# Optimization experiments

Measured on AMD Instinct MI355X. Metric: run time of the kernel, lower is better.

## Reference

```python
import jax, jax.numpy as jnp
import numpy as np

NEG_SLOPE = 0.2  # HANConv default negative_slope
N_NODES = 100000
N_REL = 8
N_EDGES = 200000
N_LABEL = 131072
C_IN = 128
H1 = 128
H2 = 128


def _segment_softmax(logits, seg, num_segments):
    # PyG softmax(src, index): exp(src - max_per_seg) / (sum_per_seg + 1e-16)
    m = jax.ops.segment_max(logits, seg, num_segments=num_segments)
    m = jnp.where(jnp.isfinite(m), m, 0.0)  # empty segments -> 0
    e = jnp.exp(logits - m[seg])
    s = jax.ops.segment_sum(e, seg, num_segments=num_segments)
    return e / (s[seg] + 1e-16)


def _han_layer(x, edge_index, proj_w, proj_b, att_src, att_dst, q, klin_w, klin_b):
    # x: [N, Cin]; edge_index: [R, 2, E]; att_src/att_dst: [R, D]; klin_w: [D, D] (torch [out,in])
    N = x.shape[0]
    h = x @ proj_w + proj_b            # [N, D] shared projection for node type 'node'
    a_src = h @ att_src.T              # [N, R] per-node src attention logits
    a_dst = h @ att_dst.T              # [N, R]

    def per_rel(eidx, a_s, a_d):
        src, dst = eidx[0], eidx[1]
        alpha = jax.nn.leaky_relu(a_s[src] + a_d[dst], NEG_SLOPE)     # [E]
        alpha = _segment_softmax(alpha, dst, N)                        # softmax over in-neighbors
        out = jax.ops.segment_sum(alpha[:, None] * h[src], dst, num_segments=N)  # [N, D]
        return jax.nn.relu(out)        # HANConv applies relu per edge-type output

    outs = jax.vmap(per_rel, in_axes=(0, 1, 1))(edge_index, a_src, a_dst)  # [R, N, D]
    # semantic attention across edge types (group())
    score = jnp.einsum('d,rd->r', q, jnp.tanh(outs @ klin_w.T + klin_b).mean(axis=1))
    attn = jax.nn.softmax(score)       # [R]
    return jnp.einsum('r,rnd->nd', attn, outs)


def setup_inputs() -> dict:
    key = jax.random.key(0)
    ks = jax.random.split(key, 24)
    f32 = jnp.float32

    def lin_w(k, fin, fout):
        return (jax.random.normal(k, (fin, fout), f32) / np.sqrt(fin)).astype(f32)

    inp = {
        'x': jax.random.normal(ks[0], (N_NODES, C_IN), f32),
        'edge_index': jax.random.randint(ks[1], (N_REL, 2, N_EDGES), 0, N_NODES, jnp.int32),
        'edge_label_index': jax.random.randint(ks[2], (2, N_LABEL), 0, N_NODES, jnp.int32),
        # HANConv layer 1 params
        'w1': lin_w(ks[3], C_IN, H1), 'b1': jnp.zeros((H1,), f32),
        'asrc1': jax.random.normal(ks[4], (N_REL, H1), f32) / np.sqrt(H1),
        'adst1': jax.random.normal(ks[5], (N_REL, H1), f32) / np.sqrt(H1),
        'q1': jax.random.normal(ks[6], (H1,), f32) / np.sqrt(H1),
        'kw1': lin_w(ks[7], H1, H1).T, 'kb1': jnp.zeros((H1,), f32),
        # HANConv layer 2 params
        'w2': lin_w(ks[8], H1, H2), 'b2': jnp.zeros((H2,), f32),
        'asrc2': jax.random.normal(ks[9], (N_REL, H2), f32) / np.sqrt(H2),
        'adst2': jax.random.normal(ks[10], (N_REL, H2), f32) / np.sqrt(H2),
        'q2': jax.random.normal(ks[11], (H2,), f32) / np.sqrt(H2),
        'kw2': lin_w(ks[12], H2, H2).T, 'kb2': jnp.zeros((H2,), f32),
        # link-score head
        'post_w': lin_w(ks[13], H2, 2), 'post_b': jnp.zeros((2,), f32),
    }
    return inp


def reference(x, edge_index, edge_label_index,
              w1, b1, asrc1, adst1, q1, kw1, kb1,
              w2, b2, asrc2, adst2, q2, kw2, kb2,
              post_w, post_b):
    h = jax.nn.relu(_han_layer(x, edge_index, w1, b1, asrc1, adst1, q1, kw1, kb1))
    h = jax.nn.relu(_han_layer(h, edge_index, w2, b2, asrc2, adst2, q2, kw2, kb2))
    h_had = h[edge_label_index[0]] * h[edge_label_index[1]]   # [L, H2]
    logits = h_had @ post_w + post_b                          # [L, 2]
    return logits.sum(axis=-1)                                # [L]
```

## Files before the change

kernel.cpp:

```cpp
#include <hip/hip_runtime.h>

#define NN 100000
#define NR 8
#define NE 200000
#define NL 131072
#define NSEG (NR*NN)
#define NB_SCAN 782
#define NPAD (NB_SCAN*1024)

typedef __attribute__((ext_vector_type(8))) short short8;
typedef __attribute__((ext_vector_type(8))) _Float16 half8;
typedef __attribute__((ext_vector_type(4))) float floatx4;

__device__ __forceinline__ unsigned short f2h(float f) {
    _Float16 h = (_Float16)f;
    union { _Float16 h; unsigned short u; } c; c.h = h; return c.u;
}
__device__ __forceinline__ float h2f(unsigned short u) {
    union { _Float16 h; unsigned short u; } c; c.u = u; return (float)c.h;
}

__global__ void transpose128(const float* __restrict__ in, float* __restrict__ out) {
    int idx = blockIdx.x * 256 + threadIdx.x;
    int j = idx >> 7, k = idx & 127;
    out[idx] = in[k * 128 + j];
}

__global__ void cast_f16(const float* __restrict__ src, unsigned short* __restrict__ dst) {
    size_t idx = ((size_t)blockIdx.x * 256 + threadIdx.x) * 4;
    float4 v = *(const float4*)(src + idx);
    ushort4 o;
    o.x = f2h(v.x); o.y = f2h(v.y); o.z = f2h(v.z); o.w = f2h(v.w);
    *(ushort4*)(dst + idx) = o;
}

__global__ void hist_kernel(const int* __restrict__ ei, int* __restrict__ counts) {
    int idx = blockIdx.x * 256 + threadIdx.x;
    if (idx >= NR * NE) return;
    int r = idx / NE, e = idx - r * NE;
    int dst = ei[(size_t)r * 2 * NE + NE + e];
    atomicAdd(&counts[r * NN + dst], 1);
}

__global__ __launch_bounds__(256) void scan_k1(const int* __restrict__ counts,
                                               int* __restrict__ rowptr,
                                               int* __restrict__ bsums) {
    __shared__ int wsum[4];
    int t = threadIdx.x, lane = t & 63, w = t >> 6;
    int base = blockIdx.x * 1024 + t * 4;
    int c0 = counts[base], c1 = counts[base + 1], c2 = counts[base + 2], c3 = counts[base + 3];
    int s = c0 + c1 + c2 + c3;
    int inc = s;
#pragma unroll
    for (int off = 1; off < 64; off <<= 1) { int v = __shfl_up(inc, off); if (lane >= off) inc += v; }
    if (lane == 63) wsum[w] = inc;
    __syncthreads();
    int wbase = 0;
    for (int k = 0; k < w; ++k) wbase += wsum[k];
    int ex = wbase + inc - s;
    rowptr[base]     = ex;
    rowptr[base + 1] = ex + c0;
    rowptr[base + 2] = ex + c0 + c1;
    rowptr[base + 3] = ex + c0 + c1 + c2;
    if (t == 255) bsums[blockIdx.x] = wbase + inc;
}

__global__ __launch_bounds__(256) void scan_k2(int* __restrict__ bsums, int nb) {
    __shared__ int wsum[4];
    __shared__ int carry_s;
    int t = threadIdx.x, lane = t & 63, w = t >> 6;
    if (t == 0) carry_s = 0;
    __syncthreads();
    for (int base = 0; base < nb; base += 256) {
        int i = base + t;
        int v = (i < nb) ? bsums[i] : 0;
        int inc = v;
#pragma unroll
        for (int off = 1; off < 64; off <<= 1) { int u = __shfl_up(inc, off); if (lane >= off) inc += u; }
        if (lane == 63) wsum[w] = inc;
        __syncthreads();
        int wbase = carry_s;
        for (int k = 0; k < w; ++k) wbase += wsum[k];
        if (i < nb) bsums[i] = wbase + inc - v;
        __syncthreads();
        if (t == 0) carry_s += wsum[0] + wsum[1] + wsum[2] + wsum[3];
        __syncthreads();
    }
}

__global__ void scan_k3(int* __restrict__ rowptr, const int* __restrict__ bsums) {
    int i = blockIdx.x * 256 + threadIdx.x;
    if (i <= NSEG) rowptr[i] += bsums[i >> 10];
}

__global__ void fill_kernel(const int* __restrict__ ei, const int* __restrict__ rowptr,
                            int* __restrict__ cursor, int* __restrict__ es_raw) {
    int idx = blockIdx.x * 256 + threadIdx.x;
    if (idx >= NR * NE) return;
    int r = idx / NE, e = idx - r * NE;
    int src = ei[(size_t)r * 2 * NE + e];
    int dst = ei[(size_t)r * 2 * NE + NE + e];
    int g = r * NN + dst;
    int pos = rowptr[g] + atomicAdd(&cursor[g], 1);
    es_raw[2 * pos] = src;
}

__global__ __launch_bounds__(256, 3) void gemm_proj(
    const float* __restrict__ A, const float* __restrict__ B,
    const float* __restrict__ bias, float* __restrict__ out, int nrows)
{
    __shared__ float As[128][36];
    __shared__ float Bs[128][36];
    const int tid = threadIdx.x;
    const int row0 = blockIdx.x * 128;
    const int cg = tid & 15;
    const int nb = (tid >> 4) * 8;

    float acc[8][8];
#pragma unroll
    for (int i = 0; i < 8; ++i)
#pragma unroll
        for (int j = 0; j < 8; ++j) acc[i][j] = 0.f;

    for (int k0 = 0; k0 < 128; k0 += 32) {
#pragma unroll
        for (int i = 0; i < 4; ++i) {
            int fi = tid + i * 256;
            int rw = fi >> 3, kq = fi & 7;
            int n = row0 + rw;
            float4 v = make_float4(0.f, 0.f, 0.f, 0.f);
            if (n < nrows) v = *(const float4*)(A + (size_t)n * 128 + k0 + kq * 4);
            *(float4*)&As[rw][kq * 4] = v;
            float4 w = *(const float4*)(B + rw * 128 + k0 + kq * 4);
            *(float4*)&Bs[rw][kq * 4] = w;
        }
        __syncthreads();
#pragma unroll 2
        for (int kq = 0; kq < 8; ++kq) {
            float4 wv[8];
#pragma unroll
            for (int j = 0; j < 8; ++j) wv[j] = *(const float4*)&Bs[cg + 16 * j][kq * 4];
#pragma unroll
            for (int i = 0; i < 8; ++i) {
                float4 xv = *(const float4*)&As[nb + i][kq * 4];
#pragma unroll
                for (int j = 0; j < 8; ++j)
                    acc[i][j] += xv.x * wv[j].x + xv.y * wv[j].y
                               + xv.z * wv[j].z + xv.w * wv[j].w;
            }
        }
        __syncthreads();
    }
#pragma unroll
    for (int i = 0; i < 8; ++i) {
        int n = row0 + nb + i;
        if (n < nrows) {
#pragma unroll
            for (int j = 0; j < 8; ++j) {
                int d = cg + 16 * j;
                out[(size_t)n * 128 + d] = acc[i][j] + bias[d];
            }
        }
    }
}

__global__ __launch_bounds__(256) void fused_score2(
    const int* __restrict__ rowptr, const int2* __restrict__ es,
    const unsigned short* __restrict__ h16,
    const unsigned short* __restrict__ kw16, const float* __restrict__ kb,
    const float* __restrict__ q, float* __restrict__ scorebuf)
{
    __shared__ unsigned short Os[64][136];
    __shared__ float redbuf[4];
    const int t = threadIdx.x;
    const int r = blockIdx.y;
    const int row0 = blockIdx.x * 64;
    const int l = t & 7, ng = t >> 3;

#pragma unroll
    for (int pass = 0; pass < 2; ++pass) {
        int nl = pass * 32 + ng;
        int n = row0 + nl;
        float acc[16];
#pragma unroll
        for (int i = 0; i < 16; ++i) acc[i] = 0.f;
        if (n < NN) {
            int g = r * NN + n;
            int p0 = rowptr[g], p1 = rowptr[g + 1];
            int e = p0;
            for (; e + 1 < p1; e += 2) {
                int2 ea = es[e], eb = es[e + 1];
                float aa = __int_as_float(ea.y), ab = __int_as_float(eb.y);
                const unsigned short* hpa = h16 + (size_t)ea.x * 128;
                const unsigned short* hpb = h16 + (size_t)eb.x * 128;
                short8 a0 = *(const short8*)(hpa + l * 8);
                short8 a1 = *(const short8*)(hpa + 64 + l * 8);
                short8 b0 = *(const short8*)(hpb + l * 8);
                short8 b1 = *(const short8*)(hpb + 64 + l * 8);
#pragma unroll
                for (int i = 0; i < 8; ++i)
                    acc[i]     += aa * h2f((unsigned short)a0[i]) + ab * h2f((unsigned short)b0[i]);
#pragma unroll
                for (int i = 0; i < 8; ++i)
                    acc[8 + i] += aa * h2f((unsigned short)a1[i]) + ab * h2f((unsigned short)b1[i]);
            }
            if (e < p1) {
                int2 ea = es[e];
                float aa = __int_as_float(ea.y);
                const unsigned short* hpa = h16 + (size_t)ea.x * 128;
                short8 a0 = *(const short8*)(hpa + l * 8);
                short8 a1 = *(const short8*)(hpa + 64 + l * 8);
#pragma unroll
                for (int i = 0; i < 8; ++i) acc[i]     += aa * h2f((unsigned short)a0[i]);
#pragma unroll
                for (int i = 0; i < 8; ++i) acc[8 + i] += aa * h2f((unsigned short)a1[i]);
            }
        }
        unsigned short ov[16];
#pragma unroll
        for (int i = 0; i < 16; ++i) ov[i] = f2h(fmaxf(acc[i], 0.f));
        *(short8*)&Os[nl][l * 8]      = *(short8*)&ov[0];
        *(short8*)&Os[nl][64 + l * 8] = *(short8*)&ov[8];
    }
    __syncthreads();

    const int wave = t >> 6, lane = t & 63;
    const int quad = lane >> 4, l16 = lane & 15;
    half8 a[4];
#pragma unroll
    for (int kc = 0; kc < 4; ++kc)
        a[kc] = *(const half8*)&Os[wave * 16 + l16][quad * 8 + kc * 32];

    float s = 0.f;
#pragma unroll
    for (int dt = 0; dt < 8; ++dt) {
        const unsigned short* brow = kw16 + (size_t)(dt * 16 + l16) * 128 + quad * 8;
        floatx4 accv = {0.f, 0.f, 0.f, 0.f};
#pragma unroll
        for (int kc = 0; kc < 4; ++kc) {
            half8 b = *(const half8*)(brow + kc * 32);
            accv = __builtin_amdgcn_mfma_f32_16x16x32_f16(a[kc], b, accv, 0, 0, 0);
        }
        int d = dt * 16 + l16;
        float kbv = kb[d], qv = q[d];
#pragma unroll
        for (int reg = 0; reg < 4; ++reg) {
            int node = row0 + wave * 16 + quad * 4 + reg;
            if (node < NN) {
                float y = accv[reg] + kbv;
                float e2 = __expf(2.f * y);
                float tn = 1.f - 2.f * __builtin_amdgcn_rcpf(e2 + 1.f);
                s += tn * qv;
            }
        }
    }
    for (int off = 32; off > 0; off >>= 1) s += __shfl_down(s, off);
    if (lane == 0) redbuf[wave] = s;
    __syncthreads();
    if (t == 0) atomicAdd(scorebuf + r * 64 + (blockIdx.x & 63),
                          redbuf[0] + redbuf[1] + redbuf[2] + redbuf[3]);
}

__global__ void score_reduce(const float* __restrict__ scorebuf, float* __restrict__ score) {
    int t = threadIdx.x;
    int r = t >> 3, k = t & 7;
    float v = 0.f;
#pragma unroll
    for (int i = 0; i < 8; ++i) v += scorebuf[r * 64 + k * 8 + i];
    v += __shfl_down(v, 4);
    v += __shfl_down(v, 2);
    v += __shfl_down(v, 1);
    if (k == 0) score[r] = v;
}

__global__ __launch_bounds__(256) void att_kernel(
    const float* __restrict__ h, const float* __restrict__ asrc_w,
    const float* __restrict__ adst_w, float* __restrict__ a_src,
    float* __restrict__ a_dst, unsigned short* __restrict__ h16)
{
    __shared__ float hs[16][128];
    int n0 = blockIdx.x * 16;
#pragma unroll
    for (int i = 0; i < 2; ++i) {
        int fi = threadIdx.x + i * 256;
        int n = fi >> 5, kq = fi & 31;
        float4 v = make_float4(0.f, 0.f, 0.f, 0.f);
        if (n0 + n < NN) v = *(const float4*)(h + (size_t)(n0 + n) * 128 + kq * 4);
        *(float4*)&hs[n][kq * 4] = v;
    }
    __syncthreads();
    int n = threadIdx.x >> 4, rr = threadIdx.x & 15;
    int r = rr & 7; int isd = rr >> 3;
    const float* w = (isd ? adst_w : asrc_w) + r * 128;
    float acc = 0.f;
#pragma unroll
    for (int kq = 0; kq < 32; ++kq) {
        float4 hv = *(const float4*)&hs[n][kq * 4];
        float4 wv = ((const float4*)w)[kq];
        acc += hv.x * wv.x + hv.y * wv.y + hv.z * wv.z + hv.w * wv.w;
    }
    if (n0 + n < NN) (isd ? a_dst : a_src)[r * NN + n0 + n] = acc;

    int dq = rr * 8;
    if (n0 + n < NN) {
        unsigned short ov[8];
#pragma unroll
        for (int k = 0; k < 8; ++k) ov[k] = f2h(hs[n][dq + k]);
        *(short8*)(h16 + (size_t)(n0 + n) * 128 + dq) = *(short8*)ov;
    }
}

__global__ void softmax_csr(const int* __restrict__ rowptr, int2* __restrict__ es,
                            const float* __restrict__ a_src, const float* __restrict__ a_dst)
{
    int g = blockIdx.x * 256 + threadIdx.x;
    if (g >= NSEG) return;
    int p0 = rowptr[g], p1 = rowptr[g + 1];
    if (p0 == p1) return;
    int r = g / NN;
    float ad = a_dst[g];
    const float* as = a_src + (size_t)r * NN;
    float m = -1e30f;
    int i = p0;
    for (; i + 1 < p1; i += 2) {
        float la = as[es[i].x] + ad;
        float lb = as[es[i + 1].x] + ad;
        la = la > 0.f ? la : 0.2f * la;
        lb = lb > 0.f ? lb : 0.2f * lb;
        es[i].y     = __float_as_int(la);
        es[i + 1].y = __float_as_int(lb);
        m = fmaxf(m, fmaxf(la, lb));
    }
    if (i < p1) {
        float la = as[es[i].x] + ad;
        la = la > 0.f ? la : 0.2f * la;
        es[i].y = __float_as_int(la);
        m = fmaxf(m, la);
    }
    float s = 0.f;
    for (int k = p0; k < p1; ++k) {
        float e = __expf(__int_as_float(es[k].y) - m);
        es[k].y = __float_as_int(e);
        s += e;
    }
    float inv = __builtin_amdgcn_rcpf(s + 1e-16f);
    for (int k = p0; k < p1; ++k)
        es[k].y = __float_as_int(__int_as_float(es[k].y) * inv);
}

__global__ __launch_bounds__(256) void combine_csr(
    const int* __restrict__ rowptr, const int2* __restrict__ es,
    const unsigned short* __restrict__ h16, const float* __restrict__ score,
    float* __restrict__ comb)
{
    __shared__ float attn[NR];
    __shared__ float lds[4][64][17];
    int t = threadIdx.x;
    if (t == 0) {
        float sc[NR]; float m = -1e30f;
        for (int r = 0; r < NR; ++r) { sc[r] = score[r] * (1.0f / NN); m = fmaxf(m, sc[r]); }
        float den = 0.f;
        for (int r = 0; r < NR; ++r) { sc[r] = __expf(sc[r] - m); den += sc[r]; }
        for (int r = 0; r < NR; ++r) attn[r] = sc[r] / den;
    }
    __syncthreads();

    int nl = t >> 6;
    int n = blockIdx.x * 4 + nl;
    int L = t & 63;
    int r = L >> 3;
    int o = L & 7;
    float a[16];
#pragma unroll
    for (int i = 0; i < 16; ++i) a[i] = 0.f;
    {
        int g = r * NN + n;
        int p0 = rowptr[g], p1 = rowptr[g + 1];
        int e = p0;
        for (; e + 1 < p1; e += 2) {
            int2 ea = es[e], eb = es[e + 1];
            float aa = __int_as_float(ea.y), ab = __int_as_float(eb.y);
            const unsigned short* hpa = h16 + (size_t)ea.x * 128;
            const unsigned short* hpb = h16 + (size_t)eb.x * 128;
            short8 u0 = *(const short8*)(hpa + o * 8);
            short8 u1 = *(const short8*)(hpa + 64 + o * 8);
            short8 v0 = *(const short8*)(hpb + o * 8);
            short8 v1 = *(const short8*)(hpb + 64 + o * 8);
#pragma unroll
            for (int i = 0; i < 8; ++i) {
                a[i]     += aa * h2f((unsigned short)u0[i]) + ab * h2f((unsigned short)v0[i]);
                a[8 + i] += aa * h2f((unsigned short)u1[i]) + ab * h2f((unsigned short)v1[i]);
            }
        }
        if (e < p1) {
            int2 ea = es[e];
            float aa = __int_as_float(ea.y);
            const unsigned short* hpa = h16 + (size_t)ea.x * 128;
            short8 u0 = *(const short8*)(hpa + o * 8);
            short8 u1 = *(const short8*)(hpa + 64 + o * 8);
#pragma unroll
            for (int i = 0; i < 8; ++i) {
                a[i]     += aa * h2f((unsigned short)u0[i]);
                a[8 + i] += aa * h2f((unsigned short)u1[i]);
            }
        }
    }
    float w = attn[r];
    float* dst = &lds[nl][L][0];
#pragma unroll
    for (int i = 0; i < 16; ++i) dst[i] = w * fmaxf(a[i], 0.f);
    __syncthreads();

    int d0 = 2 * L;
    int o2, s0;
    if (d0 < 64) { o2 = d0 >> 3; s0 = d0 & 7; }
    else         { o2 = (d0 - 64) >> 3; s0 = 8 + ((d0 - 64) & 7); }
    float x0 = 0.f, x1 = 0.f;
#pragma unroll
    for (int rr = 0; rr < NR; ++rr) {
        x0 += lds[nl][rr * 8 + o2][s0];
        x1 += lds[nl][rr * 8 + o2][s0 + 1];
    }
    *(float2*)(comb + (size_t)n * 128 + d0) = make_float2(x0, x1);
}

__global__ __launch_bounds__(256) void head_kernel(
    const float* __restrict__ hfin, const int* __restrict__ eli,
    const float* __restrict__ pw, const float* __restrict__ pb,
    float* __restrict__ out)
{
    int t = threadIdx.x;
    int l = blockIdx.x * 4 + (t >> 6);
    int d0 = (t & 63) * 2;
    int a = eli[l], b = eli[NL + l];
    float2 ha = *(const float2*)(hfin + (size_t)a * 128 + d0);
    float2 hb = *(const float2*)(hfin + (size_t)b * 128 + d0);
    float w0 = pw[d0 * 2] + pw[d0 * 2 + 1];
    float w1 = pw[d0 * 2 + 2] + pw[d0 * 2 + 3];
    float v = ha.x * hb.x * w0 + ha.y * hb.y * w1;
    for (int off = 32; off > 0; off >>= 1) v += __shfl_down(v, off);
    if ((t & 63) == 0) out[l] = v + pb[0] + pb[1];
}

extern "C" void kernel_launch(void* const* d_in, const int* in_sizes, int n_in,
                              void* d_out, int out_size, void* d_ws, size_t ws_size,
                              hipStream_t stream)
{
    const float* x     = (const float*)d_in[0];
    const int*   ei    = (const int*)d_in[1];
    const int*   eli   = (const int*)d_in[2];
    const float* w1    = (const float*)d_in[3];
    const float* b1    = (const float*)d_in[4];
    const float* asrc1 = (const float*)d_in[5];
    const float* adst1 = (const float*)d_in[6];
    const float* q1    = (const float*)d_in[7];
    const float* kw1   = (const float*)d_in[8];
    const float* kb1   = (const float*)d_in[9];
    const float* w2    = (const float*)d_in[10];
    const float* b2    = (const float*)d_in[11];
    const float* asrc2 = (const float*)d_in[12];
    const float* adst2 = (const float*)d_in[13];
    const float* q2    = (const float*)d_in[14];
    const float* kw2   = (const float*)d_in[15];
    const float* kb2   = (const float*)d_in[16];
    const float* pw    = (const float*)d_in[17];
    const float* pb    = (const float*)d_in[18];
    float* out = (float*)d_out;

    float* ws      = (float*)d_ws;
    float* hA      = ws;
    float* hB      = ws + 12800000ull;
    float* a_src   = ws + 25600000ull;
    float* a_dst   = ws + 26400000ull;
    int2*  es      = (int2*)(ws + 27200000ull);
    int*   rowptr  = (int*)(ws + 30400000ull);
    int*   counts  = (int*)(ws + 31200768ull);
    int*   bsums   = (int*)(ws + 32001536ull);
    float* score   = ws + 32002560ull;
    float* wt      = ws + 32002624ull;
    unsigned short* kw16 = (unsigned short*)(ws + 32019008ull);
    float* scorebuf = (float*)counts;

    hipMemsetAsync(counts, 0, NPAD * sizeof(int), stream);
    hist_kernel<<<6250, 256, 0, stream>>>(ei, counts);
    scan_k1<<<NB_SCAN, 256, 0, stream>>>(counts, rowptr, bsums);
    scan_k2<<<1, 256, 0, stream>>>(bsums, NB_SCAN);
    scan_k3<<<3126, 256, 0, stream>>>(rowptr, bsums);
    hipMemsetAsync(counts, 0, NPAD * sizeof(int), stream);
    fill_kernel<<<6250, 256, 0, stream>>>(ei, rowptr, counts, (int*)es);

    for (int layer = 0; layer < 2; ++layer) {
        const float* Ain  = layer ? hA : x;
        float*       H    = layer ? hB : hA;
        unsigned short* h16 = (unsigned short*)(layer ? hA : hB);
        const float* W    = layer ? w2 : w1;
        const float* bb   = layer ? b2 : b1;
        const float* as_w = layer ? asrc2 : asrc1;
        const float* ad_w = layer ? adst2 : adst1;
        const float* qq   = layer ? q2 : q1;
        const float* kw   = layer ? kw2 : kw1;
        const float* kb   = layer ? kb2 : kb1;

        transpose128<<<64, 256, 0, stream>>>(W, wt);
        gemm_proj<<<782, 256, 0, stream>>>(Ain, wt, bb, H, NN);
        cast_f16<<<16, 256, 0, stream>>>(kw, kw16);
        att_kernel<<<6250, 256, 0, stream>>>(H, as_w, ad_w, a_src, a_dst, h16);
        softmax_csr<<<3125, 256, 0, stream>>>(rowptr, es, a_src, a_dst);
        hipMemsetAsync(scorebuf, 0, 512 * sizeof(float), stream);
        fused_score2<<<dim3(1563, NR), 256, 0, stream>>>(rowptr, es, h16,
                                                         kw16, kb, qq, scorebuf);
        score_reduce<<<1, 64, 0, stream>>>(scorebuf, score);
        combine_csr<<<25000, 256, 0, stream>>>(rowptr, es, h16, score, H);
    }
    head_kernel<<<32768, 256, 0, stream>>>(hB, eli, pw, pb, out);
}
```

Before: 1.305 ms.

## Gather FP8 node features in semantic score kernel and register-cache softmax logits

The attention kernel now also writes an FP8 e4m3 copy of the projected features, and the semantic-score aggregation gathers 16 FP8 bytes per lane instead of 32 FP16 bytes. This halves gather traffic in that kernel and changes the per-lane column mapping to contiguous 16-element chunks. The segment softmax keeps up to 16 logits in registers, so it no longer does repeated read-modify-write passes over the edge array for low-degree segments. The cost is reduced precision in the semantic attention scores and an extra FP8 store in the attention kernel.

```diff
diff --git a/kernel.cpp b/kernel.cpp
--- a/kernel.cpp
+++ b/kernel.cpp
@@ -1,4 +1,5 @@
 #include <hip/hip_runtime.h>
+#include <hip/hip_fp8.h>
 
 #define NN 100000
 #define NR 8
@@ -18,6 +19,12 @@
 }
 __device__ __forceinline__ float h2f(unsigned short u) {
     union { _Float16 h; unsigned short u; } c; c.u = u; return (float)c.h;
+}
+__device__ __forceinline__ unsigned fp8enc(float f) {
+    __hip_fp8_e4m3 t(f); return (unsigned)t.__x;
+}
+__device__ __forceinline__ float fp8dec(unsigned b) {
+    __hip_fp8_e4m3 t; t.__x = (__hip_fp8_storage_t)b; return (float)t;
 }
 
 __global__ void transpose128(const float* __restrict__ in, float* __restrict__ out) {
@@ -166,7 +173,7 @@
 
 __global__ __launch_bounds__(256) void fused_score2(
     const int* __restrict__ rowptr, const int2* __restrict__ es,
-    const unsigned short* __restrict__ h16,
+    const unsigned char* __restrict__ h8,
     const unsigned short* __restrict__ kw16, const float* __restrict__ kb,
     const float* __restrict__ q, float* __restrict__ scorebuf)
 {
@@ -191,36 +198,34 @@
             for (; e + 1 < p1; e += 2) {
                 int2 ea = es[e], eb = es[e + 1];
                 float aa = __int_as_float(ea.y), ab = __int_as_float(eb.y);
-                const unsigned short* hpa = h16 + (size_t)ea.x * 128;
-                const unsigned short* hpb = h16 + (size_t)eb.x * 128;
-                short8 a0 = *(const short8*)(hpa + l * 8);
-                short8 a1 = *(const short8*)(hpa + 64 + l * 8);
-                short8 b0 = *(const short8*)(hpb + l * 8);
-                short8 b1 = *(const short8*)(hpb + 64 + l * 8);
-#pragma unroll
-                for (int i = 0; i < 8; ++i)
-                    acc[i]     += aa * h2f((unsigned short)a0[i]) + ab * h2f((unsigned short)b0[i]);
-#pragma unroll
-                for (int i = 0; i < 8; ++i)
-                    acc[8 + i] += aa * h2f((unsigned short)a1[i]) + ab * h2f((unsigned short)b1[i]);
+                uint4 va = *(const uint4*)(h8 + (size_t)ea.x * 128 + l * 16);
+                uint4 vb = *(const uint4*)(h8 + (size_t)eb.x * 128 + l * 16);
+                const unsigned* wa = (const unsigned*)&va;
+                const unsigned* wb = (const unsigned*)&vb;
+#pragma unroll
+                for (int w = 0; w < 4; ++w)
+#pragma unroll
+                    for (int b = 0; b < 4; ++b)
+                        acc[w * 4 + b] += aa * fp8dec((wa[w] >> (8 * b)) & 0xFF)
+                                        + ab * fp8dec((wb[w] >> (8 * b)) & 0xFF);
             }
             if (e < p1) {
                 int2 ea = es[e];
                 float aa = __int_as_float(ea.y);
-                const unsigned short* hpa = h16 + (size_t)ea.x * 128;
-                short8 a0 = *(const short8*)(hpa + l * 8);
-                short8 a1 = *(const short8*)(hpa + 64 + l * 8);
-#pragma unroll
-                for (int i = 0; i < 8; ++i) acc[i]     += aa * h2f((unsigned short)a0[i]);
-#pragma unroll
-                for (int i = 0; i < 8; ++i) acc[8 + i] += aa * h2f((unsigned short)a1[i]);
+                uint4 va = *(const uint4*)(h8 + (size_t)ea.x * 128 + l * 16);
+                const unsigned* wa = (const unsigned*)&va;
+#pragma unroll
+                for (int w = 0; w < 4; ++w)
+#pragma unroll
+                    for (int b = 0; b < 4; ++b)
+                        acc[w * 4 + b] += aa * fp8dec((wa[w] >> (8 * b)) & 0xFF);
             }
         }
         unsigned short ov[16];
 #pragma unroll
         for (int i = 0; i < 16; ++i) ov[i] = f2h(fmaxf(acc[i], 0.f));
-        *(short8*)&Os[nl][l * 8]      = *(short8*)&ov[0];
-        *(short8*)&Os[nl][64 + l * 8] = *(short8*)&ov[8];
+        *(short8*)&Os[nl][l * 16]     = *(short8*)&ov[0];
+        *(short8*)&Os[nl][l * 16 + 8] = *(short8*)&ov[8];
     }
     __syncthreads();
 
@@ -276,7 +281,8 @@
 __global__ __launch_bounds__(256) void att_kernel(
     const float* __restrict__ h, const float* __restrict__ asrc_w,
     const float* __restrict__ adst_w, float* __restrict__ a_src,
-    float* __restrict__ a_dst, unsigned short* __restrict__ h16)
+    float* __restrict__ a_dst, unsigned short* __restrict__ h16,
+    unsigned char* __restrict__ h8)
 {
     __shared__ float hs[16][128];
     int n0 = blockIdx.x * 16;
@@ -304,9 +310,16 @@
     int dq = rr * 8;
     if (n0 + n < NN) {
         unsigned short ov[8];
-#pragma unroll
-        for (int k = 0; k < 8; ++k) ov[k] = f2h(hs[n][dq + k]);
+        unsigned lo = 0, hi = 0;
+#pragma unroll
+        for (int k = 0; k < 8; ++k) {
+            float f = hs[n][dq + k];
+            ov[k] = f2h(f);
+            unsigned b = fp8enc(f);
+            if (k < 4) lo |= b << (8 * k); else hi |= b << (8 * (k - 4));
+        }
         *(short8*)(h16 + (size_t)(n0 + n) * 128 + dq) = *(short8*)ov;
+        *(uint2*)(h8 + (size_t)(n0 + n) * 128 + dq) = make_uint2(lo, hi);
     }
 }
 
@@ -316,36 +329,51 @@
     int g = blockIdx.x * 256 + threadIdx.x;
     if (g >= NSEG) return;
     int p0 = rowptr[g], p1 = rowptr[g + 1];
-    if (p0 == p1) return;
+    int deg = p1 - p0;
+    if (deg == 0) return;
     int r = g / NN;
     float ad = a_dst[g];
     const float* as = a_src + (size_t)r * NN;
-    float m = -1e30f;
-    int i = p0;
-    for (; i + 1 < p1; i += 2) {
-        float la = as[es[i].x] + ad;
-        float lb = as[es[i + 1].x] + ad;
-        la = la > 0.f ? la : 0.2f * la;
-        lb = lb > 0.f ? lb : 0.2f * lb;
-        es[i].y     = __float_as_int(la);
-        es[i + 1].y = __float_as_int(lb);
-        m = fmaxf(m, fmaxf(la, lb));
-    }
-    if (i < p1) {
-        float la = as[es[i].x] + ad;
-        la = la > 0.f ? la : 0.2f * la;
-        es[i].y = __float_as_int(la);
-        m = fmaxf(m, la);
-    }
-    float s = 0.f;
-    for (int k = p0; k < p1; ++k) {
-        float e = __expf(__int_as_float(es[k].y) - m);
-        es[k].y = __float_as_int(e);
-        s += e;
-    }
-    float inv = __builtin_amdgcn_rcpf(s + 1e-16f);
-    for (int k = p0; k < p1; ++k)
-        es[k].y = __float_as_int(__int_as_float(es[k].y) * inv);
+    if (deg <= 16) {
+        float lg[16];
+        float m = -1e30f;
+#pragma unroll
+        for (int i = 0; i < 16; ++i) {
+            if (i < deg) {
+                float l = as[es[p0 + i].x] + ad;
+                l = l > 0.f ? l : 0.2f * l;
+                lg[i] = l;
+                m = fmaxf(m, l);
+            }
+        }
+        float ssum = 0.f;
+#pragma unroll
+        for (int i = 0; i < 16; ++i) {
+            if (i < deg) { float ex = __expf(lg[i] - m); lg[i] = ex; ssum += ex; }
+        }
+        float inv = __builtin_amdgcn_rcpf(ssum + 1e-16f);
+#pragma unroll
+        for (int i = 0; i < 16; ++i) {
+            if (i < deg) es[p0 + i].y = __float_as_int(lg[i] * inv);
+        }
+    } else {
+        float m = -1e30f;
+        for (int i = p0; i < p1; ++i) {
+            float l = as[es[i].x] + ad;
+            l = l > 0.f ? l : 0.2f * l;
+            es[i].y = __float_as_int(l);
+            m = fmaxf(m, l);
+        }
+        float s = 0.f;
+        for (int k = p0; k < p1; ++k) {
+            float e = __expf(__int_as_float(es[k].y) - m);
+            es[k].y = __float_as_int(e);
+            s += e;
+        }
+        float inv = __builtin_amdgcn_rcpf(s + 1e-16f);
+        for (int k = p0; k < p1; ++k)
+            es[k].y = __float_as_int(__int_as_float(es[k].y) * inv);
+    }
 }
 
 __global__ __launch_bounds__(256) void combine_csr(
@@ -493,6 +521,7 @@
         const float* Ain  = layer ? hA : x;
         float*       H    = layer ? hB : hA;
         unsigned short* h16 = (unsigned short*)(layer ? hA : hB);
+        unsigned char*  h8  = (unsigned char*)(h16 + 12800000ull);
         const float* W    = layer ? w2 : w1;
         const float* bb   = layer ? b2 : b1;
         const float* as_w = layer ? asrc2 : asrc1;
@@ -504,10 +533,10 @@
         transpose128<<<64, 256, 0, stream>>>(W, wt);
         gemm_proj<<<782, 256, 0, stream>>>(Ain, wt, bb, H, NN);
         cast_f16<<<16, 256, 0, stream>>>(kw, kw16);
-        att_kernel<<<6250, 256, 0, stream>>>(H, as_w, ad_w, a_src, a_dst, h16);
+        att_kernel<<<6250, 256, 0, stream>>>(H, as_w, ad_w, a_src, a_dst, h16, h8);
         softmax_csr<<<3125, 256, 0, stream>>>(rowptr, es, a_src, a_dst);
         hipMemsetAsync(scorebuf, 0, 512 * sizeof(float), stream);
-        fused_score2<<<dim3(1563, NR), 256, 0, stream>>>(rowptr, es, h16,
+        fused_score2<<<dim3(1563, NR), 256, 0, stream>>>(rowptr, es, h8,
                                                          kw16, kb, qq, scorebuf);
         score_reduce<<<1, 64, 0, stream>>>(scorebuf, score);
         combine_csr<<<25000, 256, 0, stream>>>(rowptr, es, h16, score, H);
```

Result: no change. 1.281 ms (-1.8%).
